# Kernel tuning notes

Measured on AMD Instinct MI355X. Metric: run time of the kernel, lower is better.

## Reference

```python
import jax, jax.numpy as jnp
import numpy as np

NUM_PINS = 10_000_000
NUM_NETS = 3_000_000


def setup_inputs() -> dict:
    key = jax.random.key(0)
    k1, k2 = jax.random.split(key)
    pos = jax.random.normal(k1, (2 * NUM_PINS,), dtype=jnp.float32) * 1000.0
    pin2net_map = jax.random.randint(k2, (NUM_PINS,), 0, NUM_NETS, dtype=jnp.int32)
    net_mask = jnp.ones((NUM_NETS,), dtype=bool)
    return {"pos": pos, "pin2net_map": pin2net_map, "net_mask": net_mask}


def reference(pos, pin2net_map, net_mask):
    # pos: [2*num_pins]; first half = x coords, second half = y coords
    num_pins = pos.shape[0] // 2
    num_nets = net_mask.shape[0]
    x = pos[:num_pins]
    y = pos[num_pins:]

    # per-net bounding box via segment min/max (the atomic scatter reduction)
    xmax = jax.ops.segment_max(x, pin2net_map, num_segments=num_nets)
    xmin = jax.ops.segment_min(x, pin2net_map, num_segments=num_nets)
    ymax = jax.ops.segment_max(y, pin2net_map, num_segments=num_nets)
    ymin = jax.ops.segment_min(y, pin2net_map, num_segments=num_nets)

    # nets with no pins would yield (-inf) - (+inf); mask them out
    counts = jax.ops.segment_sum(jnp.ones_like(x), pin2net_map, num_segments=num_nets)
    valid = net_mask & (counts > 0)

    hpwl_per_net = (xmax - xmin) + (ymax - ymin)
    total = jnp.sum(jnp.where(valid, hpwl_per_net, jnp.float32(0.0)))
    return total.reshape(1)
```

## Files before the change

### kernel.cpp

```cpp
#include <hip/hip_runtime.h>


#define BK_SHIFT 12
#define BK_NETS  4096
#define NBK_MAX  736
#define SUB      6144
#define NSUB     4
#define CHUNK    (SUB * NSUB)
#define TPB      1024
#define RTPB     512
#define CAP      20480

typedef float v4f __attribute__((ext_vector_type(4)));
typedef int   v4i __attribute__((ext_vector_type(4)));

__device__ __forceinline__ unsigned enc(float f) {
    unsigned u = __float_as_uint(f);
    return u ^ ((unsigned)((int)u >> 31) | 0x80000000u);
}
__device__ __forceinline__ float dec(unsigned u) {
    unsigned b = (u & 0x80000000u) ? (u ^ 0x80000000u) : ~u;
    return __uint_as_float(b);
}
__device__ __forceinline__ uint2 pack_rec(float x, float y, int net) {
    unsigned ex = enc(x), ey = enc(y);
    unsigned nl = (unsigned)net & (BK_NETS - 1);
    uint2 r;
    r.x = (ex & ~63u) | (nl >> 6);
    r.y = (ey & ~63u) | (nl & 63u);
    return r;
}

__device__ __forceinline__ void block_scan_excl(unsigned* arr, int n,
                                                unsigned* bufA, unsigned* bufB) {
    int t = threadIdx.x;
    unsigned v = (t < n) ? arr[t] : 0u;
    bufA[t] = v;
    __syncthreads();
    unsigned* s = bufA;
    unsigned* d = bufB;
    #pragma unroll
    for (int off = 1; off < 1024; off <<= 1) {
        unsigned x = s[t];
        if (t >= off) x += s[t - off];
        d[t] = x;
        __syncthreads();
        unsigned* tmp = s; s = d; d = tmp;
    }
    if (t < n) arr[t] = s[t] - v;
    __syncthreads();
}

__global__ __launch_bounds__(TPB) void scatter_kernel(
        const float* __restrict__ pos, const int* __restrict__ p2n,
        unsigned* __restrict__ gcur,
        uint2* __restrict__ recs,
        int P, int NBK) {
    __shared__ uint2    stage[SUB];
    __shared__ unsigned hist[NBK_MAX];
    __shared__ unsigned slab[NBK_MAX];
    __shared__ unsigned fc[NBK_MAX];
    __shared__ unsigned sstart[NBK_MAX];
    __shared__ unsigned scur[NBK_MAX];
    __shared__ unsigned scanA[1024], scanB[1024];

    const int b = blockIdx.x;
    const int pstart = b * CHUNK;
    const int pcount = min(P - pstart, CHUNK);

    for (int k = threadIdx.x; k < NBK; k += TPB) { hist[k] = 0; fc[k] = 0; }
    __syncthreads();

    int nv = pcount >> 2;
    for (int g = threadIdx.x; g < nv; g += TPB) {
        v4i n4 = *(const v4i*)(p2n + pstart + (g << 2));
        atomicAdd(&hist[n4.x >> BK_SHIFT], 1u);
        atomicAdd(&hist[n4.y >> BK_SHIFT], 1u);
        atomicAdd(&hist[n4.z >> BK_SHIFT], 1u);
        atomicAdd(&hist[n4.w >> BK_SHIFT], 1u);
    }
    __syncthreads();

    for (int k = threadIdx.x; k < NBK; k += TPB) {
        unsigned c = hist[k];
        slab[k] = c ? atomicAdd(&gcur[k], c) : 0u;
    }
    __syncthreads();

    for (int s = 0; s < NSUB; ++s) {
        int sbase = pstart + s * SUB;
        int scount = min(pcount - s * SUB, SUB);
        if (scount <= 0) break;
        int snv = scount >> 2;

        for (int k = threadIdx.x; k < NBK; k += TPB) sstart[k] = 0;
        __syncthreads();
        for (int g = threadIdx.x; g < snv; g += TPB) {
            v4i n4 = *(const v4i*)(p2n + sbase + (g << 2));
            atomicAdd(&sstart[n4.x >> BK_SHIFT], 1u);
            atomicAdd(&sstart[n4.y >> BK_SHIFT], 1u);
            atomicAdd(&sstart[n4.z >> BK_SHIFT], 1u);
            atomicAdd(&sstart[n4.w >> BK_SHIFT], 1u);
        }
        __syncthreads();
        block_scan_excl(sstart, NBK, scanA, scanB);
        for (int k = threadIdx.x; k < NBK; k += TPB) scur[k] = sstart[k];
        __syncthreads();

        for (int g = threadIdx.x; g < snv; g += TPB) {
            int p = sbase + (g << 2);
            v4i n4 = *(const v4i*)(p2n + p);
            v4f xs = __builtin_nontemporal_load((const v4f*)(pos + p));
            v4f ys = __builtin_nontemporal_load((const v4f*)(pos + P + p));
            unsigned s0 = atomicAdd(&scur[n4.x >> BK_SHIFT], 1u);
            stage[s0] = pack_rec(xs.x, ys.x, n4.x);
            unsigned s1 = atomicAdd(&scur[n4.y >> BK_SHIFT], 1u);
            stage[s1] = pack_rec(xs.y, ys.y, n4.y);
            unsigned s2 = atomicAdd(&scur[n4.z >> BK_SHIFT], 1u);
            stage[s2] = pack_rec(xs.z, ys.z, n4.z);
            unsigned s3 = atomicAdd(&scur[n4.w >> BK_SHIFT], 1u);
            stage[s3] = pack_rec(xs.w, ys.w, n4.w);
        }
        __syncthreads();

        int wid = threadIdx.x >> 6, lane = threadIdx.x & 63, nw = TPB >> 6;
        for (int bk = wid; bk < NBK; bk += nw) {
            unsigned st = sstart[bk];
            unsigned cnt = scur[bk] - st;
            unsigned base = slab[bk] + fc[bk];
            size_t dst = (size_t)bk * CAP + base;
            for (unsigned j = lane; j < cnt; j += 64)
                if (base + j < CAP)
                    recs[dst + j] = stage[st + j];
            if (lane == 0) fc[bk] += cnt;
        }
        __syncthreads();
    }
}

__global__ __launch_bounds__(RTPB) void reduce_kernel(
        const uint2* __restrict__ recs,
        const unsigned* __restrict__ gcur,
        const int* __restrict__ mask,
        float* __restrict__ out, int num_nets) {
    int k = blockIdx.x;
    __shared__ unsigned tile[4 * BK_NETS];
    for (int i = threadIdx.x; i < 4 * BK_NETS; i += RTPB) tile[i] = 0;
    __syncthreads();

    unsigned cnt = min(gcur[k], (unsigned)CAP);
    const uint2* base = recs + (size_t)k * CAP;
    const uint4* b4 = (const uint4*)base;
    unsigned nv = cnt >> 1;
    for (unsigned i = threadIdx.x; i < nv; i += RTPB) {
        uint4 q = b4[i];
        unsigned nl0 = ((q.x & 63u) << 6) | (q.y & 63u);
        unsigned ex0 = q.x & ~63u, ey0 = q.y & ~63u;
        atomicMax(&tile[nl0], ex0);
        atomicMax(&tile[BK_NETS + nl0], (~ex0) & ~63u);
        atomicMax(&tile[2 * BK_NETS + nl0], ey0);
        atomicMax(&tile[3 * BK_NETS + nl0], (~ey0) & ~63u);
        unsigned nl1 = ((q.z & 63u) << 6) | (q.w & 63u);
        unsigned ex1 = q.z & ~63u, ey1 = q.w & ~63u;
        atomicMax(&tile[nl1], ex1);
        atomicMax(&tile[BK_NETS + nl1], (~ex1) & ~63u);
        atomicMax(&tile[2 * BK_NETS + nl1], ey1);
        atomicMax(&tile[3 * BK_NETS + nl1], (~ey1) & ~63u);
    }
    if ((cnt & 1u) && threadIdx.x == 0) {
        uint2 r = base[cnt - 1];
        unsigned nl = ((r.x & 63u) << 6) | (r.y & 63u);
        unsigned ex = r.x & ~63u, ey = r.y & ~63u;
        atomicMax(&tile[nl], ex);
        atomicMax(&tile[BK_NETS + nl], (~ex) & ~63u);
        atomicMax(&tile[2 * BK_NETS + nl], ey);
        atomicMax(&tile[3 * BK_NETS + nl], (~ey) & ~63u);
    }
    __syncthreads();

    int gbase = k << BK_SHIFT;
    int nthis = min(BK_NETS, num_nets - gbase);
    float h = 0.0f;
    for (int n = threadIdx.x; n < nthis; n += RTPB) {
        unsigned a = tile[n];
        if (a != 0u && mask[gbase + n] != 0) {
            float xmax = dec(a);
            float xmin = dec(~tile[BK_NETS + n]);
            float ymax = dec(tile[2 * BK_NETS + n]);
            float ymin = dec(~tile[3 * BK_NETS + n]);
            h += (xmax - xmin) + (ymax - ymin);
        }
    }
    #pragma unroll
    for (int off = 32; off > 0; off >>= 1)
        h += __shfl_down(h, off);
    __syncthreads();
    float* ws = (float*)tile;
    int wid2 = threadIdx.x >> 6;
    if ((threadIdx.x & 63) == 0) ws[wid2] = h;
    __syncthreads();
    if (threadIdx.x == 0) {
        float t = 0.0f;
        #pragma unroll
        for (int w = 0; w < RTPB / 64; ++w) t += ws[w];
        atomicAdd(out, t);
    }
}

__device__ __forceinline__ void upd(unsigned* __restrict__ nets,
                                    float x, float y, int net) {
    unsigned ex = enc(x), ey = enc(y);
    unsigned* base = nets + ((size_t)net << 2);
    atomicMax(base + 0, ex);
    atomicMax(base + 1, ~ex);
    atomicMax(base + 2, ey);
    atomicMax(base + 3, ~ey);
}

__global__ void fb_pin_kernel(const float* __restrict__ pos,
                              const int* __restrict__ p2n,
                              unsigned* __restrict__ nets, int num_pins) {
    int i = blockIdx.x * blockDim.x + threadIdx.x;
    if (i >= num_pins) return;
    upd(nets, pos[i], pos[i + num_pins], p2n[i]);
}

__global__ void fb_net_kernel(const uint4* __restrict__ nets,
                              const int* __restrict__ mask,
                              float* __restrict__ out, int num_nets) {
    int i = blockIdx.x * blockDim.x + threadIdx.x;
    float h = 0.0f;
    if (i < num_nets) {
        uint4 v = nets[i];
        if (v.x != 0u && mask[i] != 0)
            h = (dec(v.x) - dec(~v.y)) + (dec(v.z) - dec(~v.w));
    }
    #pragma unroll
    for (int off = 32; off > 0; off >>= 1)
        h += __shfl_down(h, off);
    __shared__ float s[4];
    int wid = threadIdx.x >> 6;
    if ((threadIdx.x & 63) == 0) s[wid] = h;
    __syncthreads();
    if (threadIdx.x == 0)
        atomicAdd(out, s[0] + s[1] + s[2] + s[3]);
}

extern "C" void kernel_launch(void* const* d_in, const int* in_sizes, int n_in,
                              void* d_out, int out_size, void* d_ws, size_t ws_size,
                              hipStream_t stream) {
    const float* pos = (const float*)d_in[0];
    const int* p2n = (const int*)d_in[1];
    const int* mask = (const int*)d_in[2];
    const int P = in_sizes[0] / 2;
    const int N = in_sizes[2];

    const int NBK = (N + BK_NETS - 1) >> BK_SHIFT;
    const int NB = (P + CHUNK - 1) / CHUNK;

    size_t recs_bytes = (size_t)NBK * CAP * sizeof(uint2);
    size_t need = recs_bytes + (size_t)NBK * sizeof(unsigned) + 256;

    hipMemsetAsync(d_out, 0, sizeof(float), stream);

    size_t mean_load = (NBK > 0) ? (size_t)P / (size_t)NBK : 0;
    size_t slack = 8 * (size_t)(__builtin_sqrt((double)(mean_load + 1))) + 512;
    bool cap_ok = (NBK > 0) && (mean_load + slack <= CAP);

    if (NBK > 0 && NBK <= NBK_MAX && (P & 3) == 0 && ws_size >= need && cap_ok) {
        uint2* recs = (uint2*)d_ws;
        unsigned* gcur = (unsigned*)((char*)d_ws + recs_bytes);
        hipMemsetAsync(gcur, 0, (size_t)NBK * sizeof(unsigned), stream);

        scatter_kernel<<<NB, TPB, 0, stream>>>(pos, p2n, gcur, recs, P, NBK);
        reduce_kernel<<<NBK, RTPB, 0, stream>>>(recs, gcur, mask, (float*)d_out, N);
    } else {
        unsigned* nets = (unsigned*)d_ws;
        hipMemsetAsync(d_ws, 0, (size_t)N * 4 * sizeof(unsigned), stream);
        fb_pin_kernel<<<(P + 255) / 256, 256, 0, stream>>>(pos, p2n, nets, P);
        fb_net_kernel<<<(N + 255) / 256, 256, 0, stream>>>((const uint4*)nets, mask,
                                                           (float*)d_out, N);
    }
}
```

Measured before the change: 262.6 us.

## Reuse per-sub-chunk histograms, use wave-shuffle scan, and flatten the staged copy-out

```diff
diff --git a/kernel.cpp b/kernel.cpp
--- a/kernel.cpp
+++ b/kernel.cpp
@@ -4,12 +4,13 @@
 #define BK_SHIFT 12
 #define BK_NETS  4096
 #define NBK_MAX  736
-#define SUB      6144
-#define NSUB     4
+#define SUB      4096
+#define NSUB     6
 #define CHUNK    (SUB * NSUB)
 #define TPB      1024
-#define RTPB     512
-#define CAP      20480
+#define RTPB     1024
+#define CAP      16384
+#define CAP_SHIFT 14
 
 typedef float v4f __attribute__((ext_vector_type(4)));
 typedef int   v4i __attribute__((ext_vector_type(4)));
@@ -31,59 +32,44 @@
     return r;
 }
 
-__device__ __forceinline__ void block_scan_excl(unsigned* arr, int n,
-                                                unsigned* bufA, unsigned* bufB) {
-    int t = threadIdx.x;
-    unsigned v = (t < n) ? arr[t] : 0u;
-    bufA[t] = v;
-    __syncthreads();
-    unsigned* s = bufA;
-    unsigned* d = bufB;
-    #pragma unroll
-    for (int off = 1; off < 1024; off <<= 1) {
-        unsigned x = s[t];
-        if (t >= off) x += s[t - off];
-        d[t] = x;
-        __syncthreads();
-        unsigned* tmp = s; s = d; d = tmp;
-    }
-    if (t < n) arr[t] = s[t] - v;
-    __syncthreads();
-}
-
 __global__ __launch_bounds__(TPB) void scatter_kernel(
         const float* __restrict__ pos, const int* __restrict__ p2n,
         unsigned* __restrict__ gcur,
         uint2* __restrict__ recs,
         int P, int NBK) {
-    __shared__ uint2    stage[SUB];
-    __shared__ unsigned hist[NBK_MAX];
-    __shared__ unsigned slab[NBK_MAX];
-    __shared__ unsigned fc[NBK_MAX];
-    __shared__ unsigned sstart[NBK_MAX];
-    __shared__ unsigned scur[NBK_MAX];
-    __shared__ unsigned scanA[1024], scanB[1024];
+    __shared__ uint2          stage[SUB];
+    __shared__ unsigned short sbk[SUB];
+    __shared__ unsigned       hist4[NSUB * NBK_MAX];
+    __shared__ unsigned       slab[NBK_MAX];
+    __shared__ unsigned       fc[NBK_MAX];
+    __shared__ unsigned       sstart[NBK_MAX];
+    __shared__ unsigned       scur[NBK_MAX];
+    __shared__ unsigned       wsum[TPB / 64];
 
     const int b = blockIdx.x;
     const int pstart = b * CHUNK;
     const int pcount = min(P - pstart, CHUNK);
 
-    for (int k = threadIdx.x; k < NBK; k += TPB) { hist[k] = 0; fc[k] = 0; }
+    for (int k = threadIdx.x; k < NSUB * NBK_MAX; k += TPB) hist4[k] = 0;
     __syncthreads();
 
     int nv = pcount >> 2;
     for (int g = threadIdx.x; g < nv; g += TPB) {
         v4i n4 = *(const v4i*)(p2n + pstart + (g << 2));
-        atomicAdd(&hist[n4.x >> BK_SHIFT], 1u);
-        atomicAdd(&hist[n4.y >> BK_SHIFT], 1u);
-        atomicAdd(&hist[n4.z >> BK_SHIFT], 1u);
-        atomicAdd(&hist[n4.w >> BK_SHIFT], 1u);
+        unsigned* h = &hist4[(g >> 10) * NBK_MAX];
+        atomicAdd(&h[n4.x >> BK_SHIFT], 1u);
+        atomicAdd(&h[n4.y >> BK_SHIFT], 1u);
+        atomicAdd(&h[n4.z >> BK_SHIFT], 1u);
+        atomicAdd(&h[n4.w >> BK_SHIFT], 1u);
     }
     __syncthreads();
 
     for (int k = threadIdx.x; k < NBK; k += TPB) {
-        unsigned c = hist[k];
+        unsigned c = 0;
+        #pragma unroll
+        for (int s = 0; s < NSUB; ++s) c += hist4[s * NBK_MAX + k];
         slab[k] = c ? atomicAdd(&gcur[k], c) : 0u;
+        fc[k] = 0;
     }
     __syncthreads();
 
@@ -92,49 +78,68 @@
         int scount = min(pcount - s * SUB, SUB);
         if (scount <= 0) break;
         int snv = scount >> 2;
-
-        for (int k = threadIdx.x; k < NBK; k += TPB) sstart[k] = 0;
-        __syncthreads();
-        for (int g = threadIdx.x; g < snv; g += TPB) {
-            v4i n4 = *(const v4i*)(p2n + sbase + (g << 2));
-            atomicAdd(&sstart[n4.x >> BK_SHIFT], 1u);
-            atomicAdd(&sstart[n4.y >> BK_SHIFT], 1u);
-            atomicAdd(&sstart[n4.z >> BK_SHIFT], 1u);
-            atomicAdd(&sstart[n4.w >> BK_SHIFT], 1u);
-        }
-        __syncthreads();
-        block_scan_excl(sstart, NBK, scanA, scanB);
-        for (int k = threadIdx.x; k < NBK; k += TPB) scur[k] = sstart[k];
-        __syncthreads();
+        const unsigned* hs = &hist4[s * NBK_MAX];
+
+        {
+            int t = threadIdx.x;
+            unsigned v = (t < NBK) ? hs[t] : 0u;
+            unsigned x = v;
+            #pragma unroll
+            for (int off = 1; off < 64; off <<= 1) {
+                unsigned y = __shfl_up(x, (unsigned)off);
+                if ((t & 63) >= off) x += y;
+            }
+            if ((t & 63) == 63) wsum[t >> 6] = x;
+            __syncthreads();
+            if (t < 64) {
+                unsigned w = (t < (TPB / 64)) ? wsum[t] : 0u;
+                unsigned xx = w;
+                #pragma unroll
+                for (int off = 1; off < (TPB / 64); off <<= 1) {
+                    unsigned y = __shfl_up(xx, (unsigned)off);
+                    if (t >= off) xx += y;
+                }
+                if (t < (TPB / 64)) wsum[t] = xx - w;
+            }
+            __syncthreads();
+            if (t < NBK) {
+                unsigned e = x - v + wsum[t >> 6];
+                sstart[t] = e;
+                scur[t] = e;
+            }
+            __syncthreads();
+        }
 
         for (int g = threadIdx.x; g < snv; g += TPB) {
             int p = sbase + (g << 2);
             v4i n4 = *(const v4i*)(p2n + p);
             v4f xs = __builtin_nontemporal_load((const v4f*)(pos + p));
             v4f ys = __builtin_nontemporal_load((const v4f*)(pos + P + p));
-            unsigned s0 = atomicAdd(&scur[n4.x >> BK_SHIFT], 1u);
-            stage[s0] = pack_rec(xs.x, ys.x, n4.x);
-            unsigned s1 = atomicAdd(&scur[n4.y >> BK_SHIFT], 1u);
-            stage[s1] = pack_rec(xs.y, ys.y, n4.y);
-            unsigned s2 = atomicAdd(&scur[n4.z >> BK_SHIFT], 1u);
-            stage[s2] = pack_rec(xs.z, ys.z, n4.z);
-            unsigned s3 = atomicAdd(&scur[n4.w >> BK_SHIFT], 1u);
-            stage[s3] = pack_rec(xs.w, ys.w, n4.w);
+            int b0 = n4.x >> BK_SHIFT;
+            unsigned s0 = atomicAdd(&scur[b0], 1u);
+            stage[s0] = pack_rec(xs.x, ys.x, n4.x); sbk[s0] = (unsigned short)b0;
+            int b1 = n4.y >> BK_SHIFT;
+            unsigned s1 = atomicAdd(&scur[b1], 1u);
+            stage[s1] = pack_rec(xs.y, ys.y, n4.y); sbk[s1] = (unsigned short)b1;
+            int b2 = n4.z >> BK_SHIFT;
+            unsigned s2 = atomicAdd(&scur[b2], 1u);
+            stage[s2] = pack_rec(xs.z, ys.z, n4.z); sbk[s2] = (unsigned short)b2;
+            int b3 = n4.w >> BK_SHIFT;
+            unsigned s3 = atomicAdd(&scur[b3], 1u);
+            stage[s3] = pack_rec(xs.w, ys.w, n4.w); sbk[s3] = (unsigned short)b3;
         }
         __syncthreads();
 
-        int wid = threadIdx.x >> 6, lane = threadIdx.x & 63, nw = TPB >> 6;
-        for (int bk = wid; bk < NBK; bk += nw) {
-            unsigned st = sstart[bk];
-            unsigned cnt = scur[bk] - st;
-            unsigned base = slab[bk] + fc[bk];
-            size_t dst = (size_t)bk * CAP + base;
-            for (unsigned j = lane; j < cnt; j += 64)
-                if (base + j < CAP)
-                    recs[dst + j] = stage[st + j];
-            if (lane == 0) fc[bk] += cnt;
+        for (int i = threadIdx.x; i < scount; i += TPB) {
+            uint2 r = stage[i];
+            int bk = sbk[i];
+            unsigned off = slab[bk] + fc[bk] + ((unsigned)i - sstart[bk]);
+            if (off < CAP)
+                recs[((size_t)bk << CAP_SHIFT) + off] = r;
         }
         __syncthreads();
+
+        for (int k = threadIdx.x; k < NBK; k += TPB) fc[k] += hs[k];
     }
 }
 
@@ -149,7 +154,7 @@
     __syncthreads();
 
     unsigned cnt = min(gcur[k], (unsigned)CAP);
-    const uint2* base = recs + (size_t)k * CAP;
+    const uint2* base = recs + ((size_t)k << CAP_SHIFT);
     const uint4* b4 = (const uint4*)base;
     unsigned nv = cnt >> 1;
     for (unsigned i = threadIdx.x; i < nv; i += RTPB) {
```

Result: faster. 225.8 us (-14.0%).
